# Kernel optimization log

Measured on AMD Instinct MI355X. Metric: run time of the kernel, lower is better.

## Reference

```python
import jax, jax.numpy as jnp
import numpy as np

DEPTH = 3  # args.depth (chemprop default)


def setup_inputs() -> dict:
    key = jax.random.key(0)
    ks = jax.random.split(key, 10)
    n_atoms, n_bonds, max_nb, n_mols = 100000, 200000, 6, 4000
    H, AF, BF = 300, 133, 147  # hidden_size, atom_fdim, bond_fdim

    f_atoms = jax.random.normal(ks[0], (n_atoms, AF), jnp.float32)
    f_bonds = jax.random.normal(ks[1], (n_bonds, BF), jnp.float32)
    a2b = jax.random.randint(ks[2], (n_atoms, max_nb), 0, n_bonds)      # incoming bonds per atom
    b2a = jax.random.randint(ks[3], (n_bonds,), 0, n_atoms)             # source atom per bond
    b2revb = jax.random.randint(ks[4], (n_bonds,), 0, n_bonds)          # reverse bond index
    atom_mol = jnp.sort(jax.random.randint(ks[5], (n_atoms,), 0, n_mols))  # contiguous mol segments (a_scope)

    # Learned params (W_i, W_h bias-free per args.bias=False; W_o has bias)
    W_i = jax.random.normal(ks[6], (BF, H), jnp.float32) * (1.0 / np.sqrt(BF))
    W_h = jax.random.normal(ks[7], (H, H), jnp.float32) * (1.0 / np.sqrt(H))
    W_o = jax.random.normal(ks[8], (AF + H, H), jnp.float32) * (1.0 / np.sqrt(AF + H))
    b_o = jax.random.normal(ks[9], (H,), jnp.float32) * 0.01

    return dict(f_atoms=f_atoms, f_bonds=f_bonds, W_i=W_i, W_h=W_h, W_o=W_o, b_o=b_o,
                a2b=a2b, b2a=b2a, b2revb=b2revb, atom_mol=atom_mol, n_mols=n_mols)


def reference(f_atoms, f_bonds, W_i, W_h, W_o, b_o, a2b, b2a, b2revb, atom_mol, n_mols):
    # Bond-message D-MPNN (atom_messages=False), ReLU activation, dropout=0 (eval)
    inp = f_bonds @ W_i                       # [n_bonds, H]
    message = jax.nn.relu(inp)
    for _ in range(DEPTH - 1):
        nei_a_message = message[a2b]          # [n_atoms, max_nb, H] gather
        a_message = nei_a_message.sum(axis=1) # [n_atoms, H]
        message = a_message[b2a] - message[b2revb]  # [n_bonds, H]
        message = jax.nn.relu(inp + message @ W_h)
    # Atom readout
    a_message = message[a2b].sum(axis=1)      # [n_atoms, H]
    a_input = jnp.concatenate([f_atoms, a_message], axis=1)
    atom_hiddens = jax.nn.relu(a_input @ W_o + b_o)  # [n_atoms, H]
    # Per-molecule mean aggregation (a_scope loop -> segment ops)
    sums = jax.ops.segment_sum(atom_hiddens, atom_mol, num_segments=n_mols)
    counts = jax.ops.segment_sum(jnp.ones((atom_hiddens.shape[0],), atom_hiddens.dtype),
                                 atom_mol, num_segments=n_mols)
    return sums / jnp.maximum(counts, 1.0)[:, None]  # empty mols -> zero vector
```

## Files before the change

### kernel.cpp

```cpp
#include <hip/hip_runtime.h>
#include <hip/hip_bf16.h>
#include <stdint.h>


#define H_DIM 300
#define HP 320
#define AF_DIM 133
#define BF_DIM 147
#define MAXNB 6

typedef __hip_bfloat16 bf16;
typedef __attribute__((ext_vector_type(8))) short short8;
typedef __attribute__((ext_vector_type(4))) float f32x4;

__device__ __forceinline__ float b2f_raw(unsigned short u) {
    union { unsigned int i; float f; } v; v.i = ((unsigned int)u) << 16; return v.f;
}
__device__ __forceinline__ unsigned short f2b_raw(float f) {
    union { float f; unsigned int i; } v; v.f = f;
    unsigned int x = v.i;
    x += 0x7fffu + ((x >> 16) & 1u);
    return (unsigned short)(x >> 16);
}

__device__ __forceinline__ void gload16(const void* g, void* l) {
    __builtin_amdgcn_global_load_lds(
        (const __attribute__((address_space(1))) unsigned int*)g,
        (__attribute__((address_space(3))) unsigned int*)l,
        16, 0, 0);
}

__global__ __launch_bounds__(256) void prep_wt(
    const float* __restrict__ s1, int r1,
    const float* __restrict__ s2, int r2,
    unsigned short* __restrict__ Wt, int nkt)
{
    const int Ktot = nkt * 32;
    const int idx = blockIdx.x * 256 + threadIdx.x;
    if (idx >= 320 * Ktot) return;
    const int n = idx % 320;
    const int k = idx / 320;
    float v = 0.f;
    if (n < H_DIM) {
        if (k < 320) { if (k < r1) v = s1[k * H_DIM + n]; }
        else { const int kk = k - 320; if (kk < r2) v = s2[kk * H_DIM + n]; }
    }
    Wt[n * Ktot + k] = f2b_raw(v);
}

__global__ __launch_bounds__(256) void prep_cvt(
    const float* __restrict__ in, int W,
    unsigned short* __restrict__ outb, int ostride, int CH, int M)
{
    const int idx = blockIdx.x * 256 + threadIdx.x;
    if (idx >= M * CH) return;
    const int r = idx / CH;
    const int cc = idx - r * CH;
    uint4 o;
    unsigned short* op = (unsigned short*)&o;
#pragma unroll
    for (int j = 0; j < 8; ++j) {
        const int k = cc * 8 + j;
        op[j] = (k < W) ? f2b_raw(in[(long)r * W + k]) : 0;
    }
    *(uint4*)(outb + (long)r * ostride + cc * 8) = o;
}

template <int NKT2, int ASTR, bool RELU_A, bool BIAS_RELU>
__global__ __launch_bounds__(256) void mfma_gemm(
    const unsigned short* __restrict__ Ab,
    const unsigned short* __restrict__ Wt,
    const float* __restrict__ bias,
    bf16* __restrict__ out,
    int M)
{
    constexpr int KTOT = NKT2 * 64;

    __shared__ char As[2][2][64 * 64];
    __shared__ char Cs[16 * 640];

    const int t    = threadIdx.x;
    const int m0   = blockIdx.x * 64;
    const int wc   = t >> 6;
    const int lane = t & 63;
    const int l16  = lane & 15;
    const int quad = lane >> 4;

    const int am = t >> 2;
    const int c  = t & 3;
    const int gm = min(m0 + am, M - 1);
    const unsigned short* const agp = Ab + (long)gm * ASTR + c * 8;
    char* const d0s0 = As[0][0] + t * 16;
    char* const d0s1 = As[0][1] + t * 16;
    char* const d1s0 = As[1][0] + t * 16;
    char* const d1s1 = As[1][1] + t * 16;

    auto stage = [&](int kt, int buf) {
        const unsigned short* g = agp + kt * 64;
        gload16(g,      buf ? d1s0 : d0s0);
        gload16(g + 32, buf ? d1s1 : d0s1);
    };

    auto load_b = [&](int kt, int s, short8* bfr) {
        const int kbase = kt * 64 + s * 32 + quad * 8;
#pragma unroll
        for (int nt = 0; nt < 5; ++nt) {
            const int nn = wc * 80 + nt * 16 + l16;
            bfr[nt] = *(const short8*)(Wt + (long)nn * KTOT + kbase);
        }
    };

    f32x4 acc[4][5];
#pragma unroll
    for (int i = 0; i < 4; ++i)
#pragma unroll
        for (int j = 0; j < 5; ++j) acc[i][j] = (f32x4){0.f, 0.f, 0.f, 0.f};

    stage(0, 0);
    __syncthreads();

    for (int kt = 0; kt < NKT2; ++kt) {
        const char* const abase = (kt & 1) ? As[1][0] : As[0][0];
        short8 b0[5];
        load_b(kt, 0, b0);
        if (kt + 1 < NKT2) stage(kt + 1, (kt + 1) & 1);
        short8 afr[4];
#pragma unroll
        for (int mt = 0; mt < 4; ++mt) {
            short8 v = *(const short8*)(abase + (mt * 16 + l16) * 64 + quad * 16);
            if (RELU_A) {
                unsigned short* rp = (unsigned short*)&v;
#pragma unroll
                for (int j = 0; j < 8; ++j) rp[j] = (rp[j] & 0x8000u) ? 0 : rp[j];
            }
            afr[mt] = v;
        }
#pragma unroll
        for (int nt = 0; nt < 5; ++nt)
#pragma unroll
            for (int mt = 0; mt < 4; ++mt)
                acc[mt][nt] = __builtin_amdgcn_mfma_f32_16x16x32_bf16(
                    afr[mt], b0[nt], acc[mt][nt], 0, 0, 0);
        short8 b1[5];
        load_b(kt, 1, b1);
#pragma unroll
        for (int mt = 0; mt < 4; ++mt) {
            short8 v = *(const short8*)(abase + 4096 + (mt * 16 + l16) * 64 + quad * 16);
            if (RELU_A) {
                unsigned short* rp = (unsigned short*)&v;
#pragma unroll
                for (int j = 0; j < 8; ++j) rp[j] = (rp[j] & 0x8000u) ? 0 : rp[j];
            }
            afr[mt] = v;
        }
#pragma unroll
        for (int nt = 0; nt < 5; ++nt)
#pragma unroll
            for (int mt = 0; mt < 4; ++mt)
                acc[mt][nt] = __builtin_amdgcn_mfma_f32_16x16x32_bf16(
                    afr[mt], b1[nt], acc[mt][nt], 0, 0, 0);
        __syncthreads();
    }

    for (int mt = 0; mt < 4; ++mt) {
        __syncthreads();
#pragma unroll
        for (int nt = 0; nt < 5; ++nt) {
            const int col = wc * 80 + nt * 16 + l16;
            float bv = 0.f;
            if (BIAS_RELU) bv = (col < H_DIM) ? bias[col] : 0.f;
#pragma unroll
            for (int r = 0; r < 4; ++r) {
                float v = acc[mt][nt][r] + bv;
                if (BIAS_RELU) v = fmaxf(v, 0.f);
                ((unsigned short*)Cs)[(quad * 4 + r) * HP + col] = f2b_raw(v);
            }
        }
        __syncthreads();
        const int gr0 = m0 + mt * 16;
#pragma unroll
        for (int i = 0; i < 3; ++i) {
            const int idx = i * 256 + t;
            if (idx < 640) {
                const int row = idx / 40;
                if (gr0 + row < M)
                    *(uint4*)((char*)out + (long)(gr0 + row) * 640 + (idx - row * 40) * 16)
                        = *(const uint4*)(Cs + idx * 16);
            }
        }
    }
}

__global__ __launch_bounds__(256) void gather_sum_kernel(
    const bf16* __restrict__ msg, const int* __restrict__ a2b,
    unsigned short* __restrict__ amsg, int ostride, int n_atoms)
{
    const int idx = blockIdx.x * 256 + threadIdx.x;
    if (idx >= n_atoms * (HP / 8)) return;
    const int a = idx / (HP / 8);
    const int cc = idx - a * (HP / 8);
    float s[8] = {0.f, 0.f, 0.f, 0.f, 0.f, 0.f, 0.f, 0.f};
    const int base = a * MAXNB;
#pragma unroll
    for (int j = 0; j < MAXNB; ++j) {
        const long b = a2b[base + j];
        const uint4 u = *(const uint4*)((const char*)msg + (b * HP + cc * 8) * 2);
        const unsigned short* up = (const unsigned short*)&u;
#pragma unroll
        for (int e = 0; e < 8; ++e) s[e] += b2f_raw(up[e]);
    }
    uint4 r;
    unsigned short* rp = (unsigned short*)&r;
#pragma unroll
    for (int e = 0; e < 8; ++e) rp[e] = f2b_raw(s[e]);
    *(uint4*)(amsg + (long)a * ostride + cc * 8) = r;
}

__global__ __launch_bounds__(256) void combine_kernel(
    const bf16* __restrict__ inp, const bf16* __restrict__ Gh,
    const bf16* __restrict__ Hm, const int* __restrict__ b2a,
    const int* __restrict__ b2revb, bf16* __restrict__ outm, int n_bonds)
{
    const int idx = blockIdx.x * 256 + threadIdx.x;
    if (idx >= n_bonds * (HP / 8)) return;
    const int b = idx / (HP / 8);
    const int cc = idx - b * (HP / 8);
    const long co = (long)cc * 16;
    const long ra = b2a[b];
    const long rb = b2revb[b];
    const uint4 vi = *(const uint4*)((const char*)inp + (long)b * 640 + co);
    const uint4 vg = *(const uint4*)((const char*)Gh + ra * 640 + co);
    const uint4 vh = *(const uint4*)((const char*)Hm + rb * 640 + co);
    const unsigned short* ip = (const unsigned short*)&vi;
    const unsigned short* gp = (const unsigned short*)&vg;
    const unsigned short* hp = (const unsigned short*)&vh;
    uint4 r;
    unsigned short* rp = (unsigned short*)&r;
#pragma unroll
    for (int e = 0; e < 8; ++e) {
        const float v = b2f_raw(ip[e]) + b2f_raw(gp[e]) - b2f_raw(hp[e]);
        rp[e] = f2b_raw(fmaxf(v, 0.f));
    }
    *(uint4*)((char*)outm + (long)b * 640 + co) = r;
}

__global__ __launch_bounds__(256) void seg_mean_kernel(
    const bf16* __restrict__ hidden, const int* __restrict__ atom_mol,
    float* __restrict__ out, int n_atoms)
{
    const int m = blockIdx.x;
    const int t = threadIdx.x;
    __shared__ int s_lo, s_hi;
    __shared__ float sb[6][320];
    if (t == 0) {
        int lo = 0, hi = n_atoms;
        while (lo < hi) { int mid = (lo + hi) >> 1; if (atom_mol[mid] < m) lo = mid + 1; else hi = mid; }
        s_lo = lo;
        int lo2 = lo; hi = n_atoms;
        while (lo2 < hi) { int mid = (lo2 + hi) >> 1; if (atom_mol[mid] < m + 1) lo2 = mid + 1; else hi = mid; }
        s_hi = lo2;
    }
    __syncthreads();
    const int lo = s_lo, hi = s_hi;
    if (t < 240) {
        const int ra = t / 40;
        const int c  = t - ra * 40;
        float s[8] = {0.f, 0.f, 0.f, 0.f, 0.f, 0.f, 0.f, 0.f};
        for (int a = lo + ra; a < hi; a += 6) {
            const uint4 u = *(const uint4*)((const char*)hidden + (long)a * 640 + c * 16);
            const unsigned short* up = (const unsigned short*)&u;
#pragma unroll
            for (int e = 0; e < 8; ++e) s[e] += b2f_raw(up[e]);
        }
#pragma unroll
        for (int e = 0; e < 8; ++e) sb[ra][c * 8 + e] = s[e];
    }
    __syncthreads();
    const float inv = 1.0f / (float)max(hi - lo, 1);
    for (int cc = t; cc < H_DIM; cc += 256) {
        float s = 0.f;
#pragma unroll
        for (int r = 0; r < 6; ++r) s += sb[r][cc];
        out[(long)m * H_DIM + cc] = s * inv;
    }
}

extern "C" void kernel_launch(void* const* d_in, const int* in_sizes, int n_in,
                              void* d_out, int out_size, void* d_ws, size_t ws_size,
                              hipStream_t stream)
{
    const float* f_atoms = (const float*)d_in[0];
    const float* f_bonds = (const float*)d_in[1];
    const float* W_i     = (const float*)d_in[2];
    const float* W_h     = (const float*)d_in[3];
    const float* W_o     = (const float*)d_in[4];
    const float* b_o     = (const float*)d_in[5];
    const int*  a2b      = (const int*)d_in[6];
    const int*  b2a      = (const int*)d_in[7];
    const int*  b2revb   = (const int*)d_in[8];
    const int*  atom_mol = (const int*)d_in[9];

    const int n_atoms = in_sizes[0] / AF_DIM;
    const int n_bonds = in_sizes[1] / BF_DIM;
    const int n_mols  = out_size / H_DIM;

    char* ws = (char*)d_ws;
    size_t off = 0;
    auto alloc = [&](size_t bytes) {
        size_t o = off; off += (bytes + 255) & ~(size_t)255; return o;
    };
    bf16* inpB = (bf16*)(ws + alloc((size_t)n_bonds * HP * 2));
    bf16* msgX = (bf16*)(ws + alloc((size_t)n_bonds * HP * 2));
    bf16* HmB  = (bf16*)(ws + alloc((size_t)n_bonds * HP * 2));
    bf16* amsg = (bf16*)(ws + alloc((size_t)n_atoms * HP * 2));
    unsigned short* Wt1 = (unsigned short*)(ws + alloc(320 * 192 * 2));
    unsigned short* WtH = (unsigned short*)(ws + alloc(320 * 320 * 2));
    unsigned short* Wt3 = (unsigned short*)(ws + alloc(320 * 512 * 2));
    unsigned short* fb16    = (unsigned short*)HmB;
    unsigned short* atomcat = (unsigned short*)inpB;
    bf16* hidden = HmB;

    const dim3 blk(256);

    prep_wt<<<(320 * 192 + 255) / 256, blk, 0, stream>>>(W_i, BF_DIM, nullptr, 0, Wt1, 6);
    prep_wt<<<(320 * 320 + 255) / 256, blk, 0, stream>>>(W_h, H_DIM, nullptr, 0, WtH, 10);
    prep_wt<<<(320 * 512 + 255) / 256, blk, 0, stream>>>(W_o + (size_t)AF_DIM * H_DIM, H_DIM,
                                                         W_o, AF_DIM, Wt3, 16);

    const int gB = (n_bonds + 63) / 64;
    const int gA = (n_atoms + 63) / 64;
    const int gG = (n_atoms * (HP / 8) + 255) / 256;
    const int gC = (n_bonds * (HP / 8) + 255) / 256;

    prep_cvt<<<(n_bonds * 24 + 255) / 256, blk, 0, stream>>>(f_bonds, BF_DIM, fb16, 192, 24, n_bonds);

    mfma_gemm<3, 192, false, false><<<gB, blk, 0, stream>>>(fb16, Wt1, nullptr, inpB, n_bonds);

    mfma_gemm<5, 320, true, false><<<gB, blk, 0, stream>>>(
        (const unsigned short*)inpB, WtH, nullptr, HmB, n_bonds);
    gather_sum_kernel<<<gG, blk, 0, stream>>>(HmB, a2b, (unsigned short*)amsg, HP, n_atoms);
    combine_kernel<<<gC, blk, 0, stream>>>(inpB, amsg, HmB, b2a, b2revb, msgX, n_bonds);

    mfma_gemm<5, 320, false, false><<<gB, blk, 0, stream>>>(
        (const unsigned short*)msgX, WtH, nullptr, HmB, n_bonds);
    gather_sum_kernel<<<gG, blk, 0, stream>>>(HmB, a2b, (unsigned short*)amsg, HP, n_atoms);
    combine_kernel<<<gC, blk, 0, stream>>>(inpB, amsg, HmB, b2a, b2revb, msgX, n_bonds);

    prep_cvt<<<(n_atoms * 24 + 255) / 256, blk, 0, stream>>>(f_atoms, AF_DIM, atomcat + 320, 512, 24, n_atoms);
    gather_sum_kernel<<<gG, blk, 0, stream>>>(msgX, a2b, atomcat, 512, n_atoms);
    mfma_gemm<8, 512, false, true><<<gA, blk, 0, stream>>>(atomcat, Wt3, b_o, hidden, n_atoms);

    seg_mean_kernel<<<n_mols, blk, 0, stream>>>(hidden, atom_mol, (float*)d_out, n_atoms);
}
```

Baseline: 1.045 ms.

## Restructure MFMA GEMM to stage weights in LDS and stream activations from registers

The GEMM kernel now uses 512-thread blocks that each cover 128 rows and half the output columns (160). The weight slice for each K chunk is staged in padded LDS. Activation rows are read straight from global memory into registers instead of being double-buffered through LDS with async loads. This swaps the data-reuse pattern: weights are reused from LDS across 8 waves, while activations are read twice, once per column half. The intent is to cut per-iteration global weight loads and raise occupancy, at the risk of doubled activation traffic and unhidden global load latency.

```diff
diff --git a/kernel.cpp b/kernel.cpp
--- a/kernel.cpp
+++ b/kernel.cpp
@@ -21,13 +21,6 @@
     unsigned int x = v.i;
     x += 0x7fffu + ((x >> 16) & 1u);
     return (unsigned short)(x >> 16);
-}
-
-__device__ __forceinline__ void gload16(const void* g, void* l) {
-    __builtin_amdgcn_global_load_lds(
-        (const __attribute__((address_space(1))) unsigned int*)g,
-        (__attribute__((address_space(3))) unsigned int*)l,
-        16, 0, 0);
 }
 
 __global__ __launch_bounds__(256) void prep_wt(
@@ -66,128 +59,89 @@
     *(uint4*)(outb + (long)r * ostride + cc * 8) = o;
 }
 
-template <int NKT2, int ASTR, bool RELU_A, bool BIAS_RELU>
-__global__ __launch_bounds__(256) void mfma_gemm(
+template <int KCHUNK, int NCHUNKS, int ASTR, bool RELU_A, bool BIAS_RELU>
+__global__ __launch_bounds__(512, 4) void mfma_gemm(
     const unsigned short* __restrict__ Ab,
     const unsigned short* __restrict__ Wt,
     const float* __restrict__ bias,
     bf16* __restrict__ out,
     int M)
 {
-    constexpr int KTOT = NKT2 * 64;
-
-    __shared__ char As[2][2][64 * 64];
-    __shared__ char Cs[16 * 640];
+    constexpr int KTOT = KCHUNK * NCHUNKS;
+    constexpr int S    = KCHUNK / 32;
+    constexpr int PSTR = KCHUNK * 2 + 16;
+    constexpr int BSZ  = 160 * PSTR;
+    constexpr int LSZ  = (BSZ > 8 * 5120) ? BSZ : 8 * 5120;
+    __shared__ char Ls[LSZ];
 
     const int t    = threadIdx.x;
-    const int m0   = blockIdx.x * 64;
-    const int wc   = t >> 6;
+    const int wave = t >> 6;
     const int lane = t & 63;
     const int l16  = lane & 15;
     const int quad = lane >> 4;
-
-    const int am = t >> 2;
-    const int c  = t & 3;
-    const int gm = min(m0 + am, M - 1);
-    const unsigned short* const agp = Ab + (long)gm * ASTR + c * 8;
-    char* const d0s0 = As[0][0] + t * 16;
-    char* const d0s1 = As[0][1] + t * 16;
-    char* const d1s0 = As[1][0] + t * 16;
-    char* const d1s1 = As[1][1] + t * 16;
-
-    auto stage = [&](int kt, int buf) {
-        const unsigned short* g = agp + kt * 64;
-        gload16(g,      buf ? d1s0 : d0s0);
-        gload16(g + 32, buf ? d1s1 : d0s1);
-    };
-
-    auto load_b = [&](int kt, int s, short8* bfr) {
-        const int kbase = kt * 64 + s * 32 + quad * 8;
-#pragma unroll
-        for (int nt = 0; nt < 5; ++nt) {
-            const int nn = wc * 80 + nt * 16 + l16;
-            bfr[nt] = *(const short8*)(Wt + (long)nn * KTOT + kbase);
+    const int rb   = blockIdx.x >> 1;
+    const int colbase = (blockIdx.x & 1) * 160;
+    const int row0 = rb * 128 + wave * 16;
+
+    const unsigned short* const aptr =
+        Ab + (long)min(row0 + l16, M - 1) * ASTR + quad * 8;
+
+    f32x4 acc[10];
+#pragma unroll
+    for (int j = 0; j < 10; ++j) acc[j] = (f32x4){0.f, 0.f, 0.f, 0.f};
+
+    for (int ch = 0; ch < NCHUNKS; ++ch) {
+        if (ch) __syncthreads();
+        constexpr int NCK = 160 * (KCHUNK / 8);
+        for (int i = t; i < NCK; i += 512) {
+            const int col = i / (KCHUNK / 8);
+            const int j   = i - col * (KCHUNK / 8);
+            const uint4 v = *(const uint4*)(Wt + (long)(colbase + col) * KTOT
+                                            + ch * KCHUNK + j * 8);
+            *(uint4*)(Ls + col * PSTR + j * 16) = v;
         }
-    };
-
-    f32x4 acc[4][5];
-#pragma unroll
-    for (int i = 0; i < 4; ++i)
-#pragma unroll
-        for (int j = 0; j < 5; ++j) acc[i][j] = (f32x4){0.f, 0.f, 0.f, 0.f};
-
-    stage(0, 0);
-    __syncthreads();
-
-    for (int kt = 0; kt < NKT2; ++kt) {
-        const char* const abase = (kt & 1) ? As[1][0] : As[0][0];
-        short8 b0[5];
-        load_b(kt, 0, b0);
-        if (kt + 1 < NKT2) stage(kt + 1, (kt + 1) & 1);
-        short8 afr[4];
-#pragma unroll
-        for (int mt = 0; mt < 4; ++mt) {
-            short8 v = *(const short8*)(abase + (mt * 16 + l16) * 64 + quad * 16);
+        __syncthreads();
+#pragma unroll
+        for (int kt = 0; kt < S; ++kt) {
+            short8 a = *(const short8*)(aptr + ch * KCHUNK + kt * 32);
             if (RELU_A) {
-                unsigned short* rp = (unsigned short*)&v;
+                unsigned short* rp = (unsigned short*)&a;
 #pragma unroll
                 for (int j = 0; j < 8; ++j) rp[j] = (rp[j] & 0x8000u) ? 0 : rp[j];
             }
-            afr[mt] = v;
-        }
-#pragma unroll
-        for (int nt = 0; nt < 5; ++nt)
-#pragma unroll
-            for (int mt = 0; mt < 4; ++mt)
-                acc[mt][nt] = __builtin_amdgcn_mfma_f32_16x16x32_bf16(
-                    afr[mt], b0[nt], acc[mt][nt], 0, 0, 0);
-        short8 b1[5];
-        load_b(kt, 1, b1);
-#pragma unroll
-        for (int mt = 0; mt < 4; ++mt) {
-            short8 v = *(const short8*)(abase + 4096 + (mt * 16 + l16) * 64 + quad * 16);
-            if (RELU_A) {
-                unsigned short* rp = (unsigned short*)&v;
-#pragma unroll
-                for (int j = 0; j < 8; ++j) rp[j] = (rp[j] & 0x8000u) ? 0 : rp[j];
-            }
-            afr[mt] = v;
-        }
-#pragma unroll
-        for (int nt = 0; nt < 5; ++nt)
-#pragma unroll
-            for (int mt = 0; mt < 4; ++mt)
-                acc[mt][nt] = __builtin_amdgcn_mfma_f32_16x16x32_bf16(
-                    afr[mt], b1[nt], acc[mt][nt], 0, 0, 0);
-        __syncthreads();
-    }
-
-    for (int mt = 0; mt < 4; ++mt) {
-        __syncthreads();
-#pragma unroll
-        for (int nt = 0; nt < 5; ++nt) {
-            const int col = wc * 80 + nt * 16 + l16;
-            float bv = 0.f;
-            if (BIAS_RELU) bv = (col < H_DIM) ? bias[col] : 0.f;
-#pragma unroll
-            for (int r = 0; r < 4; ++r) {
-                float v = acc[mt][nt][r] + bv;
-                if (BIAS_RELU) v = fmaxf(v, 0.f);
-                ((unsigned short*)Cs)[(quad * 4 + r) * HP + col] = f2b_raw(v);
+#pragma unroll
+            for (int nt = 0; nt < 10; ++nt) {
+                const short8 b = *(const short8*)(
+                    Ls + (nt * 16 + l16) * PSTR + (kt * 32 + quad * 8) * 2);
+                acc[nt] = __builtin_amdgcn_mfma_f32_16x16x32_bf16(
+                    a, b, acc[nt], 0, 0, 0);
             }
         }
-        __syncthreads();
-        const int gr0 = m0 + mt * 16;
-#pragma unroll
-        for (int i = 0; i < 3; ++i) {
-            const int idx = i * 256 + t;
-            if (idx < 640) {
-                const int row = idx / 40;
-                if (gr0 + row < M)
-                    *(uint4*)((char*)out + (long)(gr0 + row) * 640 + (idx - row * 40) * 16)
-                        = *(const uint4*)(Cs + idx * 16);
-            }
+    }
+
+    __syncthreads();
+    unsigned short* cs = (unsigned short*)(Ls + wave * 5120);
+#pragma unroll
+    for (int nt = 0; nt < 10; ++nt) {
+        const int col = colbase + nt * 16 + l16;
+        float bv = 0.f;
+        if (BIAS_RELU) bv = (col < H_DIM) ? bias[col] : 0.f;
+#pragma unroll
+        for (int r = 0; r < 4; ++r) {
+            float v = acc[nt][r] + bv;
+            if (BIAS_RELU) v = fmaxf(v, 0.f);
+            cs[(quad * 4 + r) * 160 + nt * 16 + l16] = f2b_raw(v);
         }
+    }
+#pragma unroll
+    for (int i = 0; i < 5; ++i) {
+        const int idx = i * 64 + lane;
+        const int row = idx / 20;
+        const int cj  = idx - row * 20;
+        const int grow = row0 + row;
+        if (grow < M)
+            *(uint4*)((char*)out + (long)grow * 640 + colbase * 2 + cj * 16)
+                = *(const uint4*)((char*)cs + idx * 16);
     }
 }
 
@@ -320,35 +274,35 @@
     unsigned short* atomcat = (unsigned short*)inpB;
     bf16* hidden = HmB;
 
-    const dim3 blk(256);
+    const dim3 blk(256), blkg(512);
 
     prep_wt<<<(320 * 192 + 255) / 256, blk, 0, stream>>>(W_i, BF_DIM, nullptr, 0, Wt1, 6);
     prep_wt<<<(320 * 320 + 255) / 256, blk, 0, stream>>>(W_h, H_DIM, nullptr, 0, WtH, 10);
     prep_wt<<<(320 * 512 + 255) / 256, blk, 0, stream>>>(W_o + (size_t)AF_DIM * H_DIM, H_DIM,
                                                          W_o, AF_DIM, Wt3, 16);
 
-    const int gB = (n_bonds + 63) / 64;
-    const int gA = (n_atoms + 63) / 64;
+    const int gB = ((n_bonds + 127) / 128) * 2;
+    const int gA = ((n_atoms + 127) / 128) * 2;
     const int gG = (n_atoms * (HP / 8) + 255) / 256;
     const int gC = (n_bonds * (HP / 8) + 255) / 256;
 
     prep_cvt<<<(n_bonds * 24 + 255) / 256, blk, 0, stream>>>(f_bonds, BF_DIM, fb16, 192, 24, n_bonds);
 
-    mfma_gemm<3, 192, false, false><<<gB, blk, 0, stream>>>(fb16, Wt1, nullptr, inpB, n_bonds);
-
-    mfma_gemm<5, 320, true, false><<<gB, blk, 0, stream>>>(
+    mfma_gemm<192, 1, 192, false, false><<<gB, blkg, 0, stream>>>(fb16, Wt1, nullptr, inpB, n_bonds);
+
+    mfma_gemm<160, 2, 320, true, false><<<gB, blkg, 0, stream>>>(
         (const unsigned short*)inpB, WtH, nullptr, HmB, n_bonds);
     gather_sum_kernel<<<gG, blk, 0, stream>>>(HmB, a2b, (unsigned short*)amsg, HP, n_atoms);
     combine_kernel<<<gC, blk, 0, stream>>>(inpB, amsg, HmB, b2a, b2revb, msgX, n_bonds);
 
-    mfma_gemm<5, 320, false, false><<<gB, blk, 0, stream>>>(
+    mfma_gemm<160, 2, 320, false, false><<<gB, blkg, 0, stream>>>(
         (const unsigned short*)msgX, WtH, nullptr, HmB, n_bonds);
     gather_sum_kernel<<<gG, blk, 0, stream>>>(HmB, a2b, (unsigned short*)amsg, HP, n_atoms);
     combine_kernel<<<gC, blk, 0, stream>>>(inpB, amsg, HmB, b2a, b2revb, msgX, n_bonds);
 
     prep_cvt<<<(n_atoms * 24 + 255) / 256, blk, 0, stream>>>(f_atoms, AF_DIM, atomcat + 320, 512, 24, n_atoms);
     gather_sum_kernel<<<gG, blk, 0, stream>>>(msgX, a2b, atomcat, 512, n_atoms);
-    mfma_gemm<8, 512, false, true><<<gA, blk, 0, stream>>>(atomcat, Wt3, b_o, hidden, n_atoms);
+    mfma_gemm<128, 4, 512, false, true><<<gA, blkg, 0, stream>>>(atomcat, Wt3, b_o, hidden, n_atoms);
 
     seg_mean_kernel<<<n_mols, blk, 0, stream>>>(hidden, atom_mol, (float*)d_out, n_atoms);
 }
```

New measurement: 958.0 us. 1.09x faster.
